# Performance work log

Measured on AMD Instinct MI355X. Metric: run time of the kernel, lower is better.

Reference implementation:

```python
import jax, jax.numpy as jnp
import numpy as np

N_NODES = 50000
N_EDGES = 1600000
F_IN, F_LAT, F_EMB = 128, 256, 128
N_GRAPHS = 64


def _linear_init(key, out_dim, in_dim):
    scale = 1.0 / np.sqrt(in_dim)
    return jax.random.uniform(key, (out_dim, in_dim), jnp.float32, -scale, scale)


def setup_inputs() -> dict:
    key = jax.random.key(0)
    ks = jax.random.split(key, 12)
    x = jax.random.normal(ks[0], (N_NODES, F_IN), jnp.float32)
    edge_index = jax.random.randint(ks[1], (2, N_EDGES), 0, N_NODES, jnp.int64)
    batch = jnp.sort(jax.random.randint(ks[2], (N_NODES,), 0, N_GRAPHS, jnp.int64))
    return {
        'x': x,
        'edge_index': edge_index,
        'batch': batch,
        'W1l': _linear_init(ks[3], F_LAT, F_IN),
        'b1': jnp.zeros((F_LAT,), jnp.float32),
        'W1r': _linear_init(ks[4], F_LAT, F_IN),
        'W2l': _linear_init(ks[5], F_LAT, F_LAT),
        'b2': jnp.zeros((F_LAT,), jnp.float32),
        'W2r': _linear_init(ks[6], F_LAT, F_LAT),
        'W3l': _linear_init(ks[7], F_EMB, F_LAT),
        'b3': jnp.zeros((F_EMB,), jnp.float32),
        'W3r': _linear_init(ks[8], F_EMB, F_LAT),
    }


def _sage_conv(x, src, dst, deg_inv, Wl, bl, Wr):
    # mean aggregation of neighbor features: scatter-add then divide by in-degree
    agg = jax.ops.segment_sum(x[src], dst, num_segments=N_NODES) * deg_inv
    # PyG SAGEConv: lin_l(agg) + lin_r(x); lin_l has bias, lin_r does not
    return agg @ Wl.T + bl + x @ Wr.T


def reference(x, edge_index, batch, W1l, b1, W1r, W2l, b2, W2r, W3l, b3, W3r):
    src, dst = edge_index[0], edge_index[1]
    deg = jax.ops.segment_sum(jnp.ones((N_EDGES,), jnp.float32), dst, num_segments=N_NODES)
    deg_inv = jnp.where(deg > 0, 1.0 / deg, 0.0)[:, None]  # [N,1]
    h = jax.nn.relu(_sage_conv(x, src, dst, deg_inv, W1l, b1, W1r))
    h = jax.nn.relu(_sage_conv(h, src, dst, deg_inv, W2l, b2, W2r))
    h = jax.nn.relu(_sage_conv(h, src, dst, deg_inv, W3l, b3, W3r))
    # global_add_pool: per-graph sum over nodes
    return jax.ops.segment_sum(h, batch, num_segments=N_GRAPHS)
```

## Files before the change

kernel.cpp:

```cpp
#include <hip/hip_runtime.h>
#include <hip/hip_bf16.h>

#define N_NODES 50000
#define N_EDGES 1600000
#define N_GRAPHS 64

#define NBKT 250
#define BKT_NODES 200
#define BKT_CAP 7168
#define CHUNK 2048
#define NBB 782
#define NCVX 6250
#define NCVW 256

typedef short bf16x8 __attribute__((ext_vector_type(8)));
typedef float f32x4 __attribute__((ext_vector_type(4)));
typedef float f32x2 __attribute__((ext_vector_type(2)));

__device__ __forceinline__ float bf_lo(unsigned int u) { return __uint_as_float(u << 16); }
__device__ __forceinline__ float bf_hi(unsigned int u) { return __uint_as_float(u & 0xffff0000u); }
__device__ __forceinline__ unsigned short f2bf(float f) {
    unsigned int u = __float_as_uint(f);
    u = (u + 0x7fffu + ((u >> 16) & 1u)) >> 16;
    return (unsigned short)u;
}
__device__ __forceinline__ unsigned int pack2bf(float a, float b) {
    return (unsigned int)f2bf(a) | ((unsigned int)f2bf(b) << 16);
}
__device__ __forceinline__ unsigned int pack4fp8(float a, float b, float c, float d) {
    unsigned int q = __builtin_amdgcn_cvt_pk_fp8_f32(a, b, 0, false);
    q = __builtin_amdgcn_cvt_pk_fp8_f32(c, d, q, true);
    return q;
}
__device__ __forceinline__ void load_lds16(const void* g, void* l) {
    __builtin_amdgcn_global_load_lds(
        (const __attribute__((address_space(1))) void*)g,
        (__attribute__((address_space(3))) void*)l, 16, 0, 0);
}

__global__ __launch_bounds__(256) void k_front(
    const int* __restrict__ src, const int* __restrict__ dst,
    unsigned int* __restrict__ bucketed, int* __restrict__ gcnt,
    const float* __restrict__ x, unsigned short* __restrict__ A1x,
    unsigned char* __restrict__ x8,
    const float* __restrict__ W1l, const float* __restrict__ W1r,
    const float* __restrict__ W2l, const float* __restrict__ W2r,
    const float* __restrict__ W3l, const float* __restrict__ W3r,
    unsigned short* __restrict__ Wp1, unsigned short* __restrict__ Wp2,
    unsigned short* __restrict__ Wp3) {
    const int blk = blockIdx.x;
    const int t = threadIdx.x;

    if (blk < NBB) {
        __shared__ int lcnt[256];
        __shared__ int sc[256];
        __shared__ int lscan[256];
        __shared__ int gb[256];
        __shared__ unsigned int grouped[CHUNK];

        const int base = blk * CHUNK;
        const int ccnt = min(CHUNK, N_EDGES - base);
        lcnt[t] = 0;
        __syncthreads();

        unsigned int pk[CHUNK / 256];
        int rk[CHUNK / 256];
#pragma unroll
        for (int r = 0; r < CHUNK / 256; ++r) {
            int j = r * 256 + t;
            rk[r] = -1;
            if (j < ccnt) {
                int i = base + j;
                int s = src[i];
                int d = dst[i];
                int b = d / BKT_NODES;
                int dl = d - b * BKT_NODES;
                pk[r] = (unsigned int)s | ((unsigned int)dl << 16) | ((unsigned int)b << 24);
                rk[r] = atomicAdd(&lcnt[b], 1);
            }
        }
        __syncthreads();
        sc[t] = lcnt[t];
        __syncthreads();
        for (int off = 1; off < 256; off <<= 1) {
            int v = (t >= off) ? sc[t - off] : 0;
            __syncthreads();
            sc[t] += v;
            __syncthreads();
        }
        lscan[t] = sc[t] - lcnt[t];
        if (t < NBKT && lcnt[t] > 0) gb[t] = atomicAdd(&gcnt[t], lcnt[t]);
        __syncthreads();
#pragma unroll
        for (int r = 0; r < CHUNK / 256; ++r) {
            if (rk[r] >= 0) {
                int b = pk[r] >> 24;
                grouped[lscan[b] + rk[r]] = pk[r];
            }
        }
        __syncthreads();
#pragma unroll
        for (int r = 0; r < CHUNK / 256; ++r) {
            int j = r * 256 + t;
            if (j < ccnt) {
                unsigned int v = grouped[j];
                int b = v >> 24;
                int pos = gb[b] + (j - lscan[b]);
                if (pos < BKT_CAP) bucketed[b * BKT_CAP + pos] = v;
            }
        }
    } else if (blk < NBB + NCVX) {
        int i = (blk - NBB) * 256 + t;
        int r = i >> 5;
        int f4 = (i & 31) << 2;
        float4 v = *(const float4*)&x[(size_t)r * 128 + f4];
        uint2 o;
        o.x = pack2bf(v.x, v.y);
        o.y = pack2bf(v.z, v.w);
        *(uint2*)&A1x[(size_t)r * 256 + f4] = o;
        *(unsigned int*)&x8[(size_t)r * 128 + f4] = pack4fp8(v.x, v.y, v.z, v.w);
    } else {
        int i = (blk - NBB - NCVX) * 256 + t;
        const float* srcp;
        unsigned short* dstp;
        int sf4, dstride;
        if (i < 16384) {
            int h = i >> 13;
            i &= 8191;
            srcp = h ? W1r : W1l;
            dstp = Wp1 + (h ? 128 : 0);
            sf4 = 32; dstride = 256;
        } else if (i < 49152) {
            int j = i - 16384;
            int h = j >> 14;
            i = j & 16383;
            srcp = h ? W2r : W2l;
            dstp = Wp2 + (h ? 256 : 0);
            sf4 = 64; dstride = 512;
        } else {
            int j = i - 49152;
            int h = j >> 13;
            i = j & 8191;
            srcp = h ? W3r : W3l;
            dstp = Wp3 + (h ? 128 * 256 : 0);
            sf4 = 64; dstride = 256;
        }
        int r = i / sf4;
        int f4 = (i % sf4) * 4;
        float4 v = *(const float4*)&srcp[(size_t)r * (sf4 * 4) + f4];
        uint2 o;
        o.x = pack2bf(v.x, v.y);
        o.y = pack2bf(v.z, v.w);
        *(uint2*)&dstp[(size_t)r * dstride + f4] = o;
    }
}

__global__ __launch_bounds__(256) void k_place(const unsigned int* __restrict__ bucketed,
                                               const int* __restrict__ gcnt,
                                               int* __restrict__ offs,
                                               unsigned short* __restrict__ ssrc) {
    __shared__ unsigned int ent[BKT_CAP];
    __shared__ unsigned short rks[BKT_CAP];
    __shared__ int lcnt[256];
    __shared__ int sc[256];
    __shared__ int lofs[256];
    __shared__ int excl[256];

    const int b = blockIdx.x;
    const int t = threadIdx.x;

    int gv = (t < NBKT) ? gcnt[t] : 0;
    sc[t] = gv;
    __syncthreads();
    for (int off = 1; off < 256; off <<= 1) {
        int u = (t >= off) ? sc[t - off] : 0;
        __syncthreads();
        sc[t] += u;
        __syncthreads();
    }
    excl[t] = sc[t] - gv;
    __syncthreads();
    const int gstart = excl[b];
    const int cnt = min(gcnt[b], BKT_CAP);
    if (b == 0 && t == 0) offs[N_NODES] = N_EDGES;

    const unsigned int* eg = bucketed + (size_t)b * BKT_CAP;
    lcnt[t] = 0;
    __syncthreads();
    for (int i = t; i < cnt; i += 256) {
        unsigned int v = eg[i];
        ent[i] = v;
        int dl = (v >> 16) & 0xFF;
        rks[i] = (unsigned short)atomicAdd(&lcnt[dl], 1);
    }
    __syncthreads();
    sc[t] = lcnt[t];
    __syncthreads();
    for (int off = 1; off < 256; off <<= 1) {
        int u = (t >= off) ? sc[t - off] : 0;
        __syncthreads();
        sc[t] += u;
        __syncthreads();
    }
    lofs[t] = sc[t] - lcnt[t];
    if (t < BKT_NODES) offs[b * BKT_NODES + t] = gstart + lofs[t];
    __syncthreads();
    for (int i = t; i < cnt; i += 256) {
        unsigned int v = ent[i];
        int dl = (v >> 16) & 0xFF;
        int pos = lofs[dl] + (int)rks[i];
        ssrc[gstart + pos] = (unsigned short)(v & 0xFFFF);
    }
}

__global__ __launch_bounds__(256) void k_cvt8(const unsigned short* __restrict__ in,
                                              int istride, int width,
                                              unsigned char* __restrict__ out,
                                              int total8) {
    int i = blockIdx.x * 256 + threadIdx.x;
    if (i >= total8) return;
    int w8 = width >> 3;
    int r = i / w8;
    int c8 = (i - r * w8) << 3;
    uint4 v = *(const uint4*)&in[(size_t)r * istride + c8];
    uint2 q;
    q.x = pack4fp8(bf_lo(v.x), bf_hi(v.x), bf_lo(v.y), bf_hi(v.y));
    q.y = pack4fp8(bf_lo(v.z), bf_hi(v.z), bf_lo(v.w), bf_hi(v.w));
    *(uint2*)&out[(size_t)r * width + c8] = q;
}

#define DEC_ADD(dw, base)                                             \
    {                                                                 \
        f32x2 lo_ = __builtin_amdgcn_cvt_pk_f32_fp8((dw), false);     \
        f32x2 hi_ = __builtin_amdgcn_cvt_pk_f32_fp8((dw), true);      \
        a[(base) + 0] += lo_.x;                                       \
        a[(base) + 1] += lo_.y;                                       \
        a[(base) + 2] += hi_.x;                                       \
        a[(base) + 3] += hi_.y;                                       \
    }

template <int F>
__global__ __launch_bounds__(256) void k_gather8(const unsigned char* __restrict__ in,
                                                 unsigned short* __restrict__ out,
                                                 int ostride,
                                                 const int* __restrict__ offs,
                                                 const unsigned short* __restrict__ ssrc) {
    constexpr int TPN = F / 16;
    constexpr int NPB = 256 / TPN;
    int n = blockIdx.x * NPB + threadIdx.x / TPN;
    int f16 = (threadIdx.x % TPN) * 16;
    if (n >= N_NODES) return;
    int s0 = offs[n], s1 = offs[n + 1];
    float a[16];
#pragma unroll
    for (int j = 0; j < 16; ++j) a[j] = 0.f;
    const unsigned char* inf = in + f16;
    int i = s0;
    for (; i + 4 <= s1; i += 4) {
        int e0 = ssrc[i], e1 = ssrc[i + 1], e2 = ssrc[i + 2], e3 = ssrc[i + 3];
        uint4 v0 = *(const uint4*)&inf[(size_t)e0 * F];
        uint4 v1 = *(const uint4*)&inf[(size_t)e1 * F];
        uint4 v2 = *(const uint4*)&inf[(size_t)e2 * F];
        uint4 v3 = *(const uint4*)&inf[(size_t)e3 * F];
        DEC_ADD(v0.x, 0) DEC_ADD(v0.y, 4) DEC_ADD(v0.z, 8) DEC_ADD(v0.w, 12)
        DEC_ADD(v1.x, 0) DEC_ADD(v1.y, 4) DEC_ADD(v1.z, 8) DEC_ADD(v1.w, 12)
        DEC_ADD(v2.x, 0) DEC_ADD(v2.y, 4) DEC_ADD(v2.z, 8) DEC_ADD(v2.w, 12)
        DEC_ADD(v3.x, 0) DEC_ADD(v3.y, 4) DEC_ADD(v3.z, 8) DEC_ADD(v3.w, 12)
    }
    for (; i < s1; ++i) {
        uint4 v = *(const uint4*)&inf[(size_t)ssrc[i] * F];
        DEC_ADD(v.x, 0) DEC_ADD(v.y, 4) DEC_ADD(v.z, 8) DEC_ADD(v.w, 12)
    }
    int deg = s1 - s0;
    float scl = (deg > 0) ? 1.f / (float)deg : 0.f;
    uint4 o0, o1;
    o0.x = pack2bf(a[0] * scl, a[1] * scl);
    o0.y = pack2bf(a[2] * scl, a[3] * scl);
    o0.z = pack2bf(a[4] * scl, a[5] * scl);
    o0.w = pack2bf(a[6] * scl, a[7] * scl);
    o1.x = pack2bf(a[8] * scl, a[9] * scl);
    o1.y = pack2bf(a[10] * scl, a[11] * scl);
    o1.z = pack2bf(a[12] * scl, a[13] * scl);
    o1.w = pack2bf(a[14] * scl, a[15] * scl);
    *(uint4*)&out[(size_t)n * ostride + f16] = o0;
    *(uint4*)&out[(size_t)n * ostride + f16 + 8] = o1;
}

template <int KSTEPS, bool RELU, bool BIAS>
__global__ __launch_bounds__(256) void k_gemm_mfma(const unsigned short* __restrict__ A,
                                                   const unsigned short* __restrict__ W,
                                                   const float* __restrict__ bias,
                                                   unsigned short* __restrict__ C,
                                                   int ldc, int coff, int M) {
    constexpr int K = KSTEPS * 64;
    __shared__ unsigned short As[2][128 * 64];
    __shared__ unsigned short Ws[2][128 * 64];

    const int tid = threadIdx.x;
    const int lane = tid & 63;
    const int w = tid >> 6;
    const int row0 = blockIdx.x * 128;
    const int colb = blockIdx.y * 128;

    const int srow_b = w * 32 + (lane >> 3);
    const int slot = lane & 7;

    f32x4 acc[4][4];
#pragma unroll
    for (int i = 0; i < 4; ++i)
#pragma unroll
        for (int j = 0; j < 4; ++j) acc[i][j] = (f32x4){0.f, 0.f, 0.f, 0.f};

    const int m0 = (w >> 1) * 64;
    const int n0 = (w & 1) * 64;

    auto STAGE = [&](int b, int ks) {
        const int kk0 = ks * 64;
#pragma unroll
        for (int it = 0; it < 4; ++it) {
            int r = srow_b + it * 8;
            int sl = (slot ^ (r & 7)) << 3;
            int ra = min(row0 + r, M - 1);
            load_lds16(A + (size_t)ra * K + kk0 + sl,
                       (char*)As[b] + w * 4096 + it * 1024);
            load_lds16(W + (size_t)(colb + r) * K + kk0 + sl,
                       (char*)Ws[b] + w * 4096 + it * 1024);
        }
    };

    STAGE(0, 0);
    __syncthreads();
    int cur = 0;

    for (int ks = 0; ks < KSTEPS; ++ks) {
        if (ks + 1 < KSTEPS) STAGE(cur ^ 1, ks + 1);

        bf16x8 af[4][2], bfr[4][2];
#pragma unroll
        for (int mf = 0; mf < 4; ++mf)
#pragma unroll
            for (int kk = 0; kk < 2; ++kk) {
                int r = m0 + mf * 16 + (lane & 15);
                int sl = (kk * 4 + (lane >> 4)) ^ (r & 7);
                af[mf][kk] = *(const bf16x8*)((const char*)As[cur] + r * 128 + sl * 16);
            }
#pragma unroll
        for (int nf = 0; nf < 4; ++nf)
#pragma unroll
            for (int kk = 0; kk < 2; ++kk) {
                int r = n0 + nf * 16 + (lane & 15);
                int sl = (kk * 4 + (lane >> 4)) ^ (r & 7);
                bfr[nf][kk] = *(const bf16x8*)((const char*)Ws[cur] + r * 128 + sl * 16);
            }
#pragma unroll
        for (int mf = 0; mf < 4; ++mf)
#pragma unroll
            for (int nf = 0; nf < 4; ++nf)
#pragma unroll
                for (int kk = 0; kk < 2; ++kk)
                    acc[mf][nf] = __builtin_amdgcn_mfma_f32_16x16x32_bf16(
                        af[mf][kk], bfr[nf][kk], acc[mf][nf], 0, 0, 0);
        __syncthreads();
        cur ^= 1;
    }

#pragma unroll
    for (int mf = 0; mf < 4; ++mf) {
#pragma unroll
        for (int nf = 0; nf < 4; ++nf) {
            int c = colb + n0 + nf * 16 + (lane & 15);
            float bv = 0.f;
            if constexpr (BIAS) bv = bias[c];
#pragma unroll
            for (int r = 0; r < 4; ++r) {
                int m = row0 + m0 + mf * 16 + ((lane >> 4) << 2) + r;
                if (m < M) {
                    float v = acc[mf][nf][r] + bv;
                    if constexpr (RELU) v = fmaxf(v, 0.f);
                    C[(size_t)m * ldc + coff + c] = f2bf(v);
                }
            }
        }
    }
}

__global__ __launch_bounds__(256) void k_final8(const unsigned char* __restrict__ t3l8,
                                                const unsigned short* __restrict__ t3,
                                                const float* __restrict__ b3,
                                                const int* __restrict__ offs,
                                                const unsigned short* __restrict__ ssrc,
                                                const int* __restrict__ batch,
                                                float* __restrict__ out) {
    __shared__ float sm[16][128];
    __shared__ int bsh[16];
    const int t = threadIdx.x;
    const int sub = t >> 4;
    const int f8 = (t & 15) * 8;
    const int n = blockIdx.x * 16 + sub;

    int s0 = offs[n], s1 = offs[n + 1];
    float a[8];
#pragma unroll
    for (int j = 0; j < 8; ++j) a[j] = 0.f;
    const unsigned char* inf = t3l8 + f8;
    int i = s0;
    for (; i + 4 <= s1; i += 4) {
        int e0 = ssrc[i], e1 = ssrc[i + 1], e2 = ssrc[i + 2], e3 = ssrc[i + 3];
        uint2 v0 = *(const uint2*)&inf[(size_t)e0 * 128];
        uint2 v1 = *(const uint2*)&inf[(size_t)e1 * 128];
        uint2 v2 = *(const uint2*)&inf[(size_t)e2 * 128];
        uint2 v3 = *(const uint2*)&inf[(size_t)e3 * 128];
        DEC_ADD(v0.x, 0) DEC_ADD(v0.y, 4)
        DEC_ADD(v1.x, 0) DEC_ADD(v1.y, 4)
        DEC_ADD(v2.x, 0) DEC_ADD(v2.y, 4)
        DEC_ADD(v3.x, 0) DEC_ADD(v3.y, 4)
    }
    for (; i < s1; ++i) {
        uint2 v = *(const uint2*)&inf[(size_t)ssrc[i] * 128];
        DEC_ADD(v.x, 0) DEC_ADD(v.y, 4)
    }
    int deg = s1 - s0;
    float scl = (deg > 0) ? 1.f / (float)deg : 0.f;
    float4 bv0 = *(const float4*)&b3[f8];
    float4 bv1 = *(const float4*)&b3[f8 + 4];
    uint4 tr = *(const uint4*)&t3[(size_t)n * 256 + 128 + f8];
    float tv[8] = {bf_lo(tr.x), bf_hi(tr.x), bf_lo(tr.y), bf_hi(tr.y),
                   bf_lo(tr.z), bf_hi(tr.z), bf_lo(tr.w), bf_hi(tr.w)};
    float bb[8] = {bv0.x, bv0.y, bv0.z, bv0.w, bv1.x, bv1.y, bv1.z, bv1.w};
#pragma unroll
    for (int j = 0; j < 8; ++j)
        sm[sub][f8 + j] = fmaxf(a[j] * scl + bb[j] + tv[j], 0.f);
    if ((t & 15) == 0) bsh[sub] = batch[n];
    __syncthreads();

    if (t < 128) {
        float local = 0.f;
        int cur = -1;
#pragma unroll
        for (int k = 0; k < 16; ++k) {
            int b = bsh[k];
            if (b != cur) {
                if (cur >= 0) atomicAdd(&out[(size_t)cur * 128 + t], local);
                local = 0.f;
                cur = b;
            }
            local += sm[k][t];
        }
        if (cur >= 0) atomicAdd(&out[(size_t)cur * 128 + t], local);
    }
}

extern "C" void kernel_launch(void* const* d_in, const int* in_sizes, int n_in,
                              void* d_out, int out_size, void* d_ws, size_t ws_size,
                              hipStream_t stream) {
    const float* x   = (const float*)d_in[0];
    const int* ei    = (const int*)d_in[1];
    const int* batch = (const int*)d_in[2];
    const float* W1l = (const float*)d_in[3];
    const float* b1  = (const float*)d_in[4];
    const float* W1r = (const float*)d_in[5];
    const float* W2l = (const float*)d_in[6];
    const float* b2  = (const float*)d_in[7];
    const float* W2r = (const float*)d_in[8];
    const float* W3l = (const float*)d_in[9];
    const float* b3  = (const float*)d_in[10];
    const float* W3r = (const float*)d_in[11];
    const int* src = ei;
    const int* dst = ei + N_EDGES;
    float* out = (float*)d_out;

    size_t off = 0;
    auto carve = [&](size_t bytes) {
        void* p = (char*)d_ws + off;
        off += (bytes + 255) & ~(size_t)255;
        return p;
    };
    int* gcnt   = (int*)carve(256 * 4);
    int* offs   = (int*)carve((size_t)(N_NODES + 1) * 4);
    unsigned short* ssrc = (unsigned short*)carve((size_t)N_EDGES * 2);
    unsigned short* A1   = (unsigned short*)carve((size_t)N_NODES * 256 * 2);
    unsigned short* A2   = (unsigned short*)carve((size_t)N_NODES * 512 * 2);
    unsigned short* A3   = (unsigned short*)carve((size_t)N_NODES * 256 * 2);
    void* t3region = carve((size_t)N_NODES * 256 * 2);
    unsigned int* bucketed = (unsigned int*)t3region;
    unsigned short* t3 = (unsigned short*)t3region;
    unsigned char* x8   = (unsigned char*)carve((size_t)N_NODES * 128);
    unsigned char* h18  = (unsigned char*)carve((size_t)N_NODES * 256);
    unsigned char* t3l8 = (unsigned char*)carve((size_t)N_NODES * 128);
    unsigned short* Wp1 = (unsigned short*)carve((size_t)256 * 256 * 2);
    unsigned short* Wp2 = (unsigned short*)carve((size_t)256 * 512 * 2);
    unsigned short* Wp3 = (unsigned short*)carve((size_t)256 * 256 * 2);

    hipMemsetAsync(gcnt, 0, 256 * 4, stream);
    hipMemsetAsync(d_out, 0, (size_t)out_size * 4, stream);

    k_front<<<NBB + NCVX + NCVW, 256, 0, stream>>>(src, dst, bucketed, gcnt,
                                                   x, A1 + 128, x8,
                                                   W1l, W1r, W2l, W2r, W3l, W3r,
                                                   Wp1, Wp2, Wp3);
    k_place<<<NBKT, 256, 0, stream>>>(bucketed, gcnt, offs, ssrc);

    const dim3 ggrid((N_NODES + 127) / 128, 2);

    k_gather8<128><<<(N_NODES + 31) / 32, 256, 0, stream>>>(x8, A1, 256, offs, ssrc);
    k_gemm_mfma<4, true, true><<<ggrid, 256, 0, stream>>>(A1, Wp1, b1, A2, 512, 256, N_NODES);

    k_cvt8<<<(N_NODES * 32 + 255) / 256, 256, 0, stream>>>(A2 + 256, 512, 256, h18, N_NODES * 32);
    k_gather8<256><<<(N_NODES + 15) / 16, 256, 0, stream>>>(h18, A2, 512, offs, ssrc);
    k_gemm_mfma<8, true, true><<<ggrid, 256, 0, stream>>>(A2, Wp2, b2, A3, 256, 0, N_NODES);

    k_gemm_mfma<4, false, false><<<ggrid, 256, 0, stream>>>(A3, Wp3, nullptr, t3, 256, 0, N_NODES);
    k_cvt8<<<(N_NODES * 16 + 255) / 256, 256, 0, stream>>>(t3, 256, 128, t3l8, N_NODES * 16);
    k_final8<<<N_NODES / 16, 256, 0, stream>>>(t3l8, t3, b3, offs, ssrc, batch, out);
}
```

Before: 336.3 us.

## Fuse FP8 conversion into GEMM epilogue and pad CSR rows to multiples of four

The standalone bf16-to-fp8 conversion kernels are removed. The GEMM epilogue now stages its output tile in shared memory and writes the fp8 copy directly, which saves two launches and a re-read of the activations. The placement kernel pads each node's neighbor list to a multiple of four using a zero dummy row, so the gather loops have no scalar tail. It also stores degrees separately and now runs 512-thread blocks. Other changes double the bucketing chunk size and add extra dummy-row gathers plus padded ssrc storage.

```diff
diff --git a/kernel.cpp b/kernel.cpp
--- a/kernel.cpp
+++ b/kernel.cpp
@@ -8,10 +8,11 @@
 #define NBKT 250
 #define BKT_NODES 200
 #define BKT_CAP 7168
-#define CHUNK 2048
-#define NBB 782
+#define CHUNK 4096
+#define NBB 391
 #define NCVX 6250
 #define NCVW 256
+#define ZROW N_NODES
 
 typedef short bf16x8 __attribute__((ext_vector_type(8)));
 typedef float f32x4 __attribute__((ext_vector_type(4)));
@@ -155,78 +156,73 @@
     }
 }
 
-__global__ __launch_bounds__(256) void k_place(const unsigned int* __restrict__ bucketed,
+__global__ __launch_bounds__(512) void k_place(const unsigned int* __restrict__ bucketed,
                                                const int* __restrict__ gcnt,
                                                int* __restrict__ offs,
+                                               unsigned short* __restrict__ deg,
                                                unsigned short* __restrict__ ssrc) {
     __shared__ unsigned int ent[BKT_CAP];
     __shared__ unsigned short rks[BKT_CAP];
     __shared__ int lcnt[256];
     __shared__ int sc[256];
     __shared__ int lofs[256];
-    __shared__ int excl[256];
+    __shared__ int gs;
 
     const int b = blockIdx.x;
     const int t = threadIdx.x;
 
-    int gv = (t < NBKT) ? gcnt[t] : 0;
-    sc[t] = gv;
+    if (t < 256) sc[t] = (t < NBKT) ? (gcnt[t] + 3 * BKT_NODES) : 0;
     __syncthreads();
     for (int off = 1; off < 256; off <<= 1) {
-        int u = (t >= off) ? sc[t - off] : 0;
-        __syncthreads();
-        sc[t] += u;
-        __syncthreads();
-    }
-    excl[t] = sc[t] - gv;
-    __syncthreads();
-    const int gstart = excl[b];
+        int u = 0;
+        if (t < 256 && t >= off) u = sc[t - off];
+        __syncthreads();
+        if (t < 256) sc[t] += u;
+        __syncthreads();
+    }
+    if (t == 0) gs = (b == 0) ? 0 : sc[b - 1];
+    if (t < 256) lcnt[t] = 0;
+    __syncthreads();
+
     const int cnt = min(gcnt[b], BKT_CAP);
-    if (b == 0 && t == 0) offs[N_NODES] = N_EDGES;
-
     const unsigned int* eg = bucketed + (size_t)b * BKT_CAP;
-    lcnt[t] = 0;
-    __syncthreads();
-    for (int i = t; i < cnt; i += 256) {
+    for (int i = t; i < cnt; i += 512) {
         unsigned int v = eg[i];
         ent[i] = v;
         int dl = (v >> 16) & 0xFF;
         rks[i] = (unsigned short)atomicAdd(&lcnt[dl], 1);
     }
     __syncthreads();
-    sc[t] = lcnt[t];
+    int pc = 0;
+    if (t < 256) {
+        pc = (lcnt[t] + 3) & ~3;
+        sc[t] = pc;
+    }
     __syncthreads();
     for (int off = 1; off < 256; off <<= 1) {
-        int u = (t >= off) ? sc[t - off] : 0;
-        __syncthreads();
-        sc[t] += u;
-        __syncthreads();
-    }
-    lofs[t] = sc[t] - lcnt[t];
-    if (t < BKT_NODES) offs[b * BKT_NODES + t] = gstart + lofs[t];
-    __syncthreads();
-    for (int i = t; i < cnt; i += 256) {
+        int u = 0;
+        if (t < 256 && t >= off) u = sc[t - off];
+        __syncthreads();
+        if (t < 256) sc[t] += u;
+        __syncthreads();
+    }
+    if (t < 256) lofs[t] = sc[t] - pc;
+    __syncthreads();
+    const int gstart = gs;
+    if (t < BKT_NODES) {
+        offs[b * BKT_NODES + t] = gstart + lofs[t];
+        deg[b * BKT_NODES + t] = (unsigned short)lcnt[t];
+    }
+    for (int i = t; i < cnt; i += 512) {
         unsigned int v = ent[i];
         int dl = (v >> 16) & 0xFF;
-        int pos = lofs[dl] + (int)rks[i];
-        ssrc[gstart + pos] = (unsigned short)(v & 0xFFFF);
-    }
-}
-
-__global__ __launch_bounds__(256) void k_cvt8(const unsigned short* __restrict__ in,
-                                              int istride, int width,
-                                              unsigned char* __restrict__ out,
-                                              int total8) {
-    int i = blockIdx.x * 256 + threadIdx.x;
-    if (i >= total8) return;
-    int w8 = width >> 3;
-    int r = i / w8;
-    int c8 = (i - r * w8) << 3;
-    uint4 v = *(const uint4*)&in[(size_t)r * istride + c8];
-    uint2 q;
-    q.x = pack4fp8(bf_lo(v.x), bf_hi(v.x), bf_lo(v.y), bf_hi(v.y));
-    q.y = pack4fp8(bf_lo(v.z), bf_hi(v.z), bf_lo(v.w), bf_hi(v.w));
-    *(uint2*)&out[(size_t)r * width + c8] = q;
+        ssrc[gstart + lofs[dl] + (int)rks[i]] = (unsigned short)(v & 0xFFFF);
+    }
+    if (t < BKT_NODES) {
+        int d = lcnt[t], pd = (d + 3) & ~3;
+        int base = gstart + lofs[t];
+        for (int j = d; j < pd; ++j) ssrc[base + j] = (unsigned short)ZROW;
+    }
 }
 
 #define DEC_ADD(dw, base)                                             \
@@ -244,19 +240,21 @@
                                                  unsigned short* __restrict__ out,
                                                  int ostride,
                                                  const int* __restrict__ offs,
+                                                 const unsigned short* __restrict__ deg,
                                                  const unsigned short* __restrict__ ssrc) {
     constexpr int TPN = F / 16;
     constexpr int NPB = 256 / TPN;
     int n = blockIdx.x * NPB + threadIdx.x / TPN;
     int f16 = (threadIdx.x % TPN) * 16;
     if (n >= N_NODES) return;
-    int s0 = offs[n], s1 = offs[n + 1];
+    int s0 = offs[n];
+    int d = deg[n];
+    int pd = (d + 3) & ~3;
     float a[16];
 #pragma unroll
     for (int j = 0; j < 16; ++j) a[j] = 0.f;
     const unsigned char* inf = in + f16;
-    int i = s0;
-    for (; i + 4 <= s1; i += 4) {
+    for (int i = s0; i < s0 + pd; i += 4) {
         int e0 = ssrc[i], e1 = ssrc[i + 1], e2 = ssrc[i + 2], e3 = ssrc[i + 3];
         uint4 v0 = *(const uint4*)&inf[(size_t)e0 * F];
         uint4 v1 = *(const uint4*)&inf[(size_t)e1 * F];
@@ -267,12 +265,7 @@
         DEC_ADD(v2.x, 0) DEC_ADD(v2.y, 4) DEC_ADD(v2.z, 8) DEC_ADD(v2.w, 12)
         DEC_ADD(v3.x, 0) DEC_ADD(v3.y, 4) DEC_ADD(v3.z, 8) DEC_ADD(v3.w, 12)
     }
-    for (; i < s1; ++i) {
-        uint4 v = *(const uint4*)&inf[(size_t)ssrc[i] * F];
-        DEC_ADD(v.x, 0) DEC_ADD(v.y, 4) DEC_ADD(v.z, 8) DEC_ADD(v.w, 12)
-    }
-    int deg = s1 - s0;
-    float scl = (deg > 0) ? 1.f / (float)deg : 0.f;
+    float scl = (d > 0) ? 1.f / (float)d : 0.f;
     uint4 o0, o1;
     o0.x = pack2bf(a[0] * scl, a[1] * scl);
     o0.y = pack2bf(a[2] * scl, a[3] * scl);
@@ -286,15 +279,16 @@
     *(uint4*)&out[(size_t)n * ostride + f16 + 8] = o1;
 }
 
-template <int KSTEPS, bool RELU, bool BIAS>
+template <int KSTEPS, bool RELU, bool BIAS, int FP8W>
 __global__ __launch_bounds__(256) void k_gemm_mfma(const unsigned short* __restrict__ A,
                                                    const unsigned short* __restrict__ W,
                                                    const float* __restrict__ bias,
                                                    unsigned short* __restrict__ C,
-                                                   int ldc, int coff, int M) {
+                                                   int ldc, int coff,
+                                                   unsigned char* __restrict__ fp8out,
+                                                   int M) {
     constexpr int K = KSTEPS * 64;
-    __shared__ unsigned short As[2][128 * 64];
-    __shared__ unsigned short Ws[2][128 * 64];
+    __shared__ unsigned short SH[32768];
 
     const int tid = threadIdx.x;
     const int lane = tid & 63;
@@ -322,9 +316,9 @@
             int sl = (slot ^ (r & 7)) << 3;
             int ra = min(row0 + r, M - 1);
             load_lds16(A + (size_t)ra * K + kk0 + sl,
-                       (char*)As[b] + w * 4096 + it * 1024);
+                       (char*)SH + b * 16384 + w * 4096 + it * 1024);
             load_lds16(W + (size_t)(colb + r) * K + kk0 + sl,
-                       (char*)Ws[b] + w * 4096 + it * 1024);
+                       (char*)SH + 32768 + b * 16384 + w * 4096 + it * 1024);
         }
     };
 
@@ -335,6 +329,8 @@
     for (int ks = 0; ks < KSTEPS; ++ks) {
         if (ks + 1 < KSTEPS) STAGE(cur ^ 1, ks + 1);
 
+        const char* Ab = (const char*)SH + cur * 16384;
+        const char* Wb = (const char*)SH + 32768 + cur * 16384;
         bf16x8 af[4][2], bfr[4][2];
 #pragma unroll
         for (int mf = 0; mf < 4; ++mf)
@@ -342,7 +338,7 @@
             for (int kk = 0; kk < 2; ++kk) {
                 int r = m0 + mf * 16 + (lane & 15);
                 int sl = (kk * 4 + (lane >> 4)) ^ (r & 7);
-                af[mf][kk] = *(const bf16x8*)((const char*)As[cur] + r * 128 + sl * 16);
+                af[mf][kk] = *(const bf16x8*)(Ab + r * 128 + sl * 16);
             }
 #pragma unroll
         for (int nf = 0; nf < 4; ++nf)
@@ -350,7 +346,7 @@
             for (int kk = 0; kk < 2; ++kk) {
                 int r = n0 + nf * 16 + (lane & 15);
                 int sl = (kk * 4 + (lane >> 4)) ^ (r & 7);
-                bfr[nf][kk] = *(const bf16x8*)((const char*)Ws[cur] + r * 128 + sl * 16);
+                bfr[nf][kk] = *(const bf16x8*)(Wb + r * 128 + sl * 16);
             }
 #pragma unroll
         for (int mf = 0; mf < 4; ++mf)
@@ -364,20 +360,51 @@
         cur ^= 1;
     }
 
+    const bool do8 = (FP8W > 0) && (colb < FP8W);
+
 #pragma unroll
     for (int mf = 0; mf < 4; ++mf) {
 #pragma unroll
         for (int nf = 0; nf < 4; ++nf) {
-            int c = colb + n0 + nf * 16 + (lane & 15);
+            int cl = n0 + nf * 16 + (lane & 15);
+            int c = colb + cl;
             float bv = 0.f;
             if constexpr (BIAS) bv = bias[c];
 #pragma unroll
             for (int r = 0; r < 4; ++r) {
-                int m = row0 + m0 + mf * 16 + ((lane >> 4) << 2) + r;
+                int ml = m0 + mf * 16 + ((lane >> 4) << 2) + r;
+                int m = row0 + ml;
                 if (m < M) {
                     float v = acc[mf][nf][r] + bv;
                     if constexpr (RELU) v = fmaxf(v, 0.f);
-                    C[(size_t)m * ldc + coff + c] = f2bf(v);
+                    unsigned short bf = f2bf(v);
+                    C[(size_t)m * ldc + coff + c] = bf;
+                    if constexpr (FP8W > 0)
+                        if (do8) SH[ml * 136 + cl] = bf;
+                }
+            }
+        }
+    }
+
+    if constexpr (FP8W > 0) {
+        if (do8) {
+            __syncthreads();
+#pragma unroll
+            for (int q0 = 0; q0 < 1024; q0 += 256) {
+                int q = q0 + tid;
+                int row = q >> 3;
+                int m = row0 + row;
+                if (m < M) {
+                    int cg = (q & 7) << 4;
+                    const unsigned short* tp = SH + row * 136 + cg;
+                    uint4 w0 = *(const uint4*)tp;
+                    uint4 w1 = *(const uint4*)(tp + 8);
+                    uint4 o;
+                    o.x = pack4fp8(bf_lo(w0.x), bf_hi(w0.x), bf_lo(w0.y), bf_hi(w0.y));
+                    o.y = pack4fp8(bf_lo(w0.z), bf_hi(w0.z), bf_lo(w0.w), bf_hi(w0.w));
+                    o.z = pack4fp8(bf_lo(w1.x), bf_hi(w1.x), bf_lo(w1.y), bf_hi(w1.y));
+                    o.w = pack4fp8(bf_lo(w1.z), bf_hi(w1.z), bf_lo(w1.w), bf_hi(w1.w));
+                    *(uint4*)&fp8out[(size_t)m * FP8W + colb + cg] = o;
                 }
             }
         }
@@ -388,6 +415,7 @@
                                                 const unsigned short* __restrict__ t3,
                                                 const float* __restrict__ b3,
                                                 const int* __restrict__ offs,
+                                                const unsigned short* __restrict__ deg,
                                                 const unsigned short* __restrict__ ssrc,
                                                 const int* __restrict__ batch,
                                                 float* __restrict__ out) {
@@ -398,13 +426,14 @@
     const int f8 = (t & 15) * 8;
     const int n = blockIdx.x * 16 + sub;
 
-    int s0 = offs[n], s1 = offs[n + 1];
+    int s0 = offs[n];
+    int d = deg[n];
+    int pd = (d + 3) & ~3;
     float a[8];
 #pragma unroll
     for (int j = 0; j < 8; ++j) a[j] = 0.f;
     const unsigned char* inf = t3l8 + f8;
-    int i = s0;
-    for (; i + 4 <= s1; i += 4) {
+    for (int i = s0; i < s0 + pd; i += 4) {
         int e0 = ssrc[i], e1 = ssrc[i + 1], e2 = ssrc[i + 2], e3 = ssrc[i + 3];
         uint2 v0 = *(const uint2*)&inf[(size_t)e0 * 128];
         uint2 v1 = *(const uint2*)&inf[(size_t)e1 * 128];
@@ -415,12 +444,7 @@
         DEC_ADD(v2.x, 0) DEC_ADD(v2.y, 4)
         DEC_ADD(v3.x, 0) DEC_ADD(v3.y, 4)
     }
-    for (; i < s1; ++i) {
-        uint2 v = *(const uint2*)&inf[(size_t)ssrc[i] * 128];
-        DEC_ADD(v.x, 0) DEC_ADD(v.y, 4)
-    }
-    int deg = s1 - s0;
-    float scl = (deg > 0) ? 1.f / (float)deg : 0.f;
+    float scl = (d > 0) ? 1.f / (float)d : 0.f;
     float4 bv0 = *(const float4*)&b3[f8];
     float4 bv1 = *(const float4*)&b3[f8 + 4];
     uint4 tr = *(const uint4*)&t3[(size_t)n * 256 + 128 + f8];
@@ -476,40 +500,42 @@
         return p;
     };
     int* gcnt   = (int*)carve(256 * 4);
-    int* offs   = (int*)carve((size_t)(N_NODES + 1) * 4);
-    unsigned short* ssrc = (unsigned short*)carve((size_t)N_EDGES * 2);
+    int* offs   = (int*)carve((size_t)N_NODES * 4);
+    unsigned short* deg  = (unsigned short*)carve((size_t)N_NODES * 2);
+    unsigned short* ssrc = (unsigned short*)carve((size_t)(N_EDGES + NBKT * 3 * BKT_NODES) * 2);
     unsigned short* A1   = (unsigned short*)carve((size_t)N_NODES * 256 * 2);
     unsigned short* A2   = (unsigned short*)carve((size_t)N_NODES * 512 * 2);
     unsigned short* A3   = (unsigned short*)carve((size_t)N_NODES * 256 * 2);
     void* t3region = carve((size_t)N_NODES * 256 * 2);
     unsigned int* bucketed = (unsigned int*)t3region;
     unsigned short* t3 = (unsigned short*)t3region;
-    unsigned char* x8   = (unsigned char*)carve((size_t)N_NODES * 128);
-    unsigned char* h18  = (unsigned char*)carve((size_t)N_NODES * 256);
-    unsigned char* t3l8 = (unsigned char*)carve((size_t)N_NODES * 128);
+    unsigned char* x8   = (unsigned char*)carve((size_t)(N_NODES + 1) * 128);
+    unsigned char* h18  = (unsigned char*)carve((size_t)(N_NODES + 1) * 256);
+    unsigned char* t3l8 = (unsigned char*)carve((size_t)(N_NODES + 1) * 128);
     unsigned short* Wp1 = (unsigned short*)carve((size_t)256 * 256 * 2);
     unsigned short* Wp2 = (unsigned short*)carve((size_t)256 * 512 * 2);
     unsigned short* Wp3 = (unsigned short*)carve((size_t)256 * 256 * 2);
 
     hipMemsetAsync(gcnt, 0, 256 * 4, stream);
     hipMemsetAsync(d_out, 0, (size_t)out_size * 4, stream);
+    hipMemsetAsync(x8 + (size_t)ZROW * 128, 0, 128, stream);
+    hipMemsetAsync(h18 + (size_t)ZROW * 256, 0, 256, stream);
+    hipMemsetAsync(t3l8 + (size_t)ZROW * 128, 0, 128, stream);
 
     k_front<<<NBB + NCVX + NCVW, 256, 0, stream>>>(src, dst, bucketed, gcnt,
                                                    x, A1 + 128, x8,
                                                    W1l, W1r, W2l, W2r, W3l, W3r,
                                                    Wp1, Wp2, Wp3);
-    k_place<<<NBKT, 256, 0, stream>>>(bucketed, gcnt, offs, ssrc);
+    k_place<<<NBKT, 512, 0, stream>>>(bucketed, gcnt, offs, deg, ssrc);
 
     const dim3 ggrid((N_NODES + 127) / 128, 2);
 
-    k_gather8<128><<<(N_NODES + 31) / 32, 256, 0, stream>>>(x8, A1, 256, offs, ssrc);
-    k_gemm_mfma<4, true, true><<<ggrid, 256, 0, stream>>>(A1, Wp1, b1, A2, 512, 256, N_NODES);
-
-    k_cvt8<<<(N_NODES * 32 + 255) / 256, 256, 0, stream>>>(A2 + 256, 512, 256, h18, N_NODES * 32);
-    k_gather8<256><<<(N_NODES + 15) / 16, 256, 0, stream>>>(h18, A2, 512, offs, ssrc);
-    k_gemm_mfma<8, true, true><<<ggrid, 256, 0, stream>>>(A2, Wp2, b2, A3, 256, 0, N_NODES);
-
-    k_gemm_mfma<4, false, false><<<ggrid, 256, 0, stream>>>(A3, Wp3, nullptr, t3, 256, 0, N_NODES);
-    k_cvt8<<<(N_NODES * 16 + 255) / 256, 256, 0, stream>>>(t3, 256, 128, t3l8, N_NODES * 16);
-    k_final8<<<N_NODES / 16, 256, 0, stream>>>(t3l8, t3, b3, offs, ssrc, batch, out);
-}
+    k_gather8<128><<<(N_NODES + 31) / 32, 256, 0, stream>>>(x8, A1, 256, offs, deg, ssrc);
+    k_gemm_mfma<4, true, true, 256><<<ggrid, 256, 0, stream>>>(A1, Wp1, b1, A2, 512, 256, h18, N_NODES);
+
+    k_gather8<256><<<(N_NODES + 15) / 16, 256, 0, stream>>>(h18, A2, 512, offs, deg, ssrc);
+    k_gemm_mfma<8, true, true, 0><<<ggrid, 256, 0, stream>>>(A2, Wp2, b2, A3, 256, 0, nullptr, N_NODES);
+
+    k_gemm_mfma<4, false, false, 128><<<ggrid, 256, 0, stream>>>(A3, Wp3, nullptr, t3, 256, 0, t3l8, N_NODES);
+    k_final8<<<N_NODES / 16, 256, 0, stream>>>(t3l8, t3, b3, offs, deg, ssrc, batch, out);
+}
```

After: 319.8 us. 1.05x faster.
